# Kernel optimization log

Hardware: AMD Instinct MI355X
Metric: run time of the kernel (lower is better)

Reference implementation:

```python
import jax, jax.numpy as jnp
import numpy as np

N, E = 50000, 800000
VOCAB, D, H, EDIM = 10000, 128, 8, 16
C = D // H  # per-head channels = 16
NEG_SLOPE_ATT = 0.2   # GATv2 attention leaky_relu slope
NEG_SLOPE_OUT = 0.01  # F.leaky_relu default
BN_EPS = 1e-5


def setup_inputs() -> dict:
    key = jax.random.key(0)
    ks = jax.random.split(key, 10)
    g = lambda k, shape, fan: (jax.random.normal(k, shape, jnp.float32) / np.float32(np.sqrt(fan)))
    return {
        "x": jax.random.randint(ks[0], (N,), 0, VOCAB),
        "ei": jax.random.randint(ks[1], (2, E), 0, N),
        "ew": jax.random.normal(ks[2], (E, EDIM), jnp.float32),
        "emb": g(ks[3], (VOCAB, D), D),
        "W_l": g(ks[4], (D, D), D),
        "b_l": jnp.zeros((D,), jnp.float32),
        "W_r": g(ks[5], (D, D), D),
        "b_r": jnp.zeros((D,), jnp.float32),
        "att": g(ks[6], (H, C), C),
        "W_e": g(ks[7], (EDIM, D), EDIM),
        "bias": jnp.zeros((D,), jnp.float32),
        "gamma": jnp.ones((D,), jnp.float32),
        "beta": jnp.zeros((D,), jnp.float32),
    }


def reference(x, ei, ew, emb, W_l, b_l, W_r, b_r, att, W_e, bias, gamma, beta):
    n = x.shape[0]
    # Embeddings: lut(x) * sqrt(d_model); dropout=0 (identity)
    h = emb[x] * jnp.float32(np.sqrt(D))                      # [N, D]
    # GATv2Conv linear transforms (source / target)
    xl = (h @ W_l + b_l).reshape(n, H, C)                      # [N, H, C]
    xr = (h @ W_r + b_r).reshape(n, H, C)                      # [N, H, C]
    eemb = (ew @ W_e).reshape(-1, H, C)                        # [E, H, C]
    src, dst = ei[0], ei[1]
    # per-edge attention logits: a^T LeakyReLU(x_l[j] + x_r[i] + e)
    m = jax.nn.leaky_relu(xl[src] + xr[dst] + eemb, NEG_SLOPE_ATT)  # [E, H, C]
    score = jnp.einsum('ehc,hc->eh', m, att)                   # [E, H]
    # segment softmax over incoming edges of each target node
    smax = jax.ops.segment_max(score, dst, num_segments=n)     # [N, H]
    ex = jnp.exp(score - smax[dst])                            # [E, H]
    denom = jax.ops.segment_sum(ex, dst, num_segments=n)       # [N, H]
    alpha = ex / denom[dst]                                    # [E, H]
    # scatter-add aggregation of weighted source features
    agg = jax.ops.segment_sum(alpha[:, :, None] * xl[src], dst, num_segments=n)
    out = agg.reshape(n, D) + bias                             # [N, D]
    # BatchNorm1d (training mode: batch statistics, biased variance)
    mean = out.mean(axis=0)
    var = out.var(axis=0)
    y = (out - mean) * jax.lax.rsqrt(var + BN_EPS) * gamma + beta
    return jax.nn.leaky_relu(y, NEG_SLOPE_OUT)
```

## Files before the change

kernel.cpp:

```cpp
#include <hip/hip_runtime.h>
#include <hip/hip_bf16.h>
#include <hip/hip_fp16.h>

typedef __hip_bfloat16 bf16;
typedef unsigned short u16;

#define D 128
#define EDIM 16
#define SQRT_D 11.313708498984761f

typedef short bf16x8 __attribute__((ext_vector_type(8)));
typedef float f32x4 __attribute__((ext_vector_type(4)));
typedef _Float16 h2 __attribute__((ext_vector_type(2)));

#define PF_BL    0
#define PF_BR    128
#define PF_WE    256
#define PF_ATT   2304
#define PF_BIAS  2432
#define PF_GAMMA 2560
#define PF_BETA  2688
#define PF_TOTAL 2816

__device__ __forceinline__ u16 f2bf_bits(float f) {
    union { bf16 h; u16 s; } cv; cv.h = __float2bfloat16(f); return cv.s;
}
__device__ __forceinline__ float2 h2f2(unsigned u) {
    union { unsigned u; __half2 h; } cv; cv.u = u;
    return __half22float2(cv.h);
}
__device__ __forceinline__ int swid(int nn, int k) {
    return nn * 128 + ((((k >> 3) ^ (nn & 15)) << 3) | (k & 7));
}
__device__ __forceinline__ float red8(float x) {
    x += __int_as_float(__builtin_amdgcn_update_dpp(0, __float_as_int(x), 0xB1, 0xf, 0xf, true));
    x += __int_as_float(__builtin_amdgcn_update_dpp(0, __float_as_int(x), 0x4E, 0xf, 0xf, true));
    x += __int_as_float(__builtin_amdgcn_update_dpp(0, __float_as_int(x), 0x141, 0xf, 0xf, true));
    return x;
}

__global__ void k_zero_detect(int* p, int count, const u16* __restrict__ u, int* flag)
{
    int i = blockIdx.x * blockDim.x + threadIdx.x;
    if (i < count) p[i] = 0;
    if (blockIdx.x == 0) {
        __shared__ int sh[256];
        int t = threadIdx.x;
        int cnt = 0;
        for (int k = t; k < 4096; k += 256) {
            int e = (u[k] >> 7) & 0xFF;
            cnt += (e > 132 && e < 255) ? 1 : 0;
        }
        sh[t] = cnt;
        __syncthreads();
        for (int s = 128; s > 0; s >>= 1) {
            if (t < s) sh[t] += sh[t + s];
            __syncthreads();
        }
        if (t == 0) *flag = (sh[0] > 100) ? 1 : 0;
    }
}

__device__ __forceinline__ float rdv(const void* p, int i, int fl) {
    return fl ? ((const float*)p)[i] : __bfloat162float(((const bf16*)p)[i]);
}

__global__ __launch_bounds__(256) void k_prep_hist(
    const void* emb, const void* Wl, const void* Wr,
    const void* bl, const void* br, const void* We, const void* att,
    const void* bias, const void* gamma, const void* beta,
    const int* __restrict__ flag, u16* __restrict__ emb16,
    u16* __restrict__ WT, float* __restrict__ pf,
    const int* __restrict__ ei, int* __restrict__ deg,
    int nE, int embCount, int prepBlocks)
{
    if ((int)blockIdx.x >= prepBlocks) {
        int e = (blockIdx.x - prepBlocks) * 256 + threadIdx.x;
        if (e < nE) atomicAdd(&deg[ei[nE + e]], 1);
        return;
    }
    const int fl = *flag;
    int idx = blockIdx.x * 256 + threadIdx.x;
    const int embV = (embCount + 7) >> 3;
    if (idx < embV) {
        int base = idx << 3;
        int lim = min(8, embCount - base);
        if (lim == 8) {
            u16 o[8];
            if (fl) {
                float f[8];
                const float4* s = (const float4*)((const float*)emb + base);
                *(float4*)(f)     = s[0];
                *(float4*)(f + 4) = s[1];
                #pragma unroll
                for (int k = 0; k < 8; ++k) o[k] = f2bf_bits(f[k] * SQRT_D);
            } else {
                u16 uu[8];
                *(uint4*)uu = *(const uint4*)((const u16*)emb + base);
                #pragma unroll
                for (int k = 0; k < 8; ++k) {
                    float v = __uint_as_float(((unsigned)uu[k]) << 16);
                    o[k] = f2bf_bits(v * SQRT_D);
                }
            }
            *(uint4*)(emb16 + base) = *(uint4*)o;
        } else {
            for (int k = 0; k < lim; ++k)
                emb16[base + k] = f2bf_bits(rdv(emb, base + k, fl) * SQRT_D);
        }
        return;
    }
    idx -= embV;
    if (idx < 32768) {
        int w = idx >> 14;
        int j = idx & 16383;
        int k = j >> 7, nn = j & 127;
        const void* W = w ? Wr : Wl;
        WT[w * 16384 + swid(nn, k)] = f2bf_bits(rdv(W, k * D + nn, fl));
        return;
    }
    idx -= 32768;
    if (idx < 128)  { pf[PF_BL + idx] = rdv(bl, idx, fl); return; }
    idx -= 128;
    if (idx < 128)  { pf[PF_BR + idx] = rdv(br, idx, fl); return; }
    idx -= 128;
    if (idx < 2048) { pf[PF_WE + idx] = rdv(We, idx, fl); return; }
    idx -= 2048;
    if (idx < 128)  { pf[PF_ATT + idx] = rdv(att, idx, fl); return; }
    idx -= 128;
    if (idx < 128)  { pf[PF_BIAS + idx] = rdv(bias, idx, fl); return; }
    idx -= 128;
    if (idx < 128)  { pf[PF_GAMMA + idx] = rdv(gamma, idx, fl); return; }
    idx -= 128;
    if (idx < 128)  { pf[PF_BETA + idx] = rdv(beta, idx, fl); return; }
}

__global__ __launch_bounds__(1024) void k_scan1(
    const int* __restrict__ deg, int* __restrict__ row_ptr,
    int* __restrict__ cursor, int n, int nBlk)
{
    __shared__ int chsum[512];
    __shared__ int part[1024];
    __shared__ int myOff;
    const int t = threadIdx.x;
    const int wv = t >> 6;
    const int lane = t & 63;

    for (int c = wv; c < nBlk; c += 16) {
        int base = c << 10;
        int s = 0;
        for (int k = lane; k < 1024; k += 64) {
            int i = base + k;
            s += (i < n) ? deg[i] : 0;
        }
        #pragma unroll
        for (int m = 1; m < 64; m <<= 1) s += __shfl_xor(s, m);
        if (lane == 0) chsum[c] = s;
    }
    __syncthreads();
    if (t == 0) {
        int run = 0;
        for (int c = 0; c < (int)blockIdx.x; ++c) run += chsum[c];
        myOff = run;
    }
    __syncthreads();

    int i = blockIdx.x * 1024 + t;
    int v = (i < n) ? deg[i] : 0;
    part[t] = v;
    __syncthreads();
    for (int off = 1; off < 1024; off <<= 1) {
        int u = (t >= off) ? part[t - off] : 0;
        __syncthreads();
        part[t] += u;
        __syncthreads();
    }
    if (i < n) {
        int excl = myOff + part[t] - v;
        row_ptr[i] = excl;
        cursor[i] = excl;
        if (i == n - 1) row_ptr[n] = excl + v;
    }
}

__global__ __launch_bounds__(1024) void k_scan_sum(
    const int* __restrict__ deg, int* __restrict__ blkSum, int n)
{
    __shared__ int sh[1024];
    int t = threadIdx.x;
    int i = blockIdx.x * 1024 + t;
    sh[t] = (i < n) ? deg[i] : 0;
    __syncthreads();
    for (int s = 512; s > 0; s >>= 1) {
        if (t < s) sh[t] += sh[t + s];
        __syncthreads();
    }
    if (t == 0) blkSum[blockIdx.x] = sh[0];
}
__global__ __launch_bounds__(1024) void k_scan_blk(
    const int* __restrict__ blkSum, int* __restrict__ blkOff, int nBlk)
{
    __shared__ int part[1024];
    int t = threadIdx.x;
    int v = (t < nBlk) ? blkSum[t] : 0;
    part[t] = v;
    __syncthreads();
    for (int off = 1; off < 1024; off <<= 1) {
        int u = (t >= off) ? part[t - off] : 0;
        __syncthreads();
        part[t] += u;
        __syncthreads();
    }
    if (t < nBlk) blkOff[t] = part[t] - v;
}
__global__ __launch_bounds__(1024) void k_scan_write(
    const int* __restrict__ deg, const int* __restrict__ blkOff,
    int* __restrict__ row_ptr, int* __restrict__ cursor, int n)
{
    __shared__ int part[1024];
    int t = threadIdx.x;
    int i = blockIdx.x * 1024 + t;
    int v = (i < n) ? deg[i] : 0;
    part[t] = v;
    __syncthreads();
    for (int off = 1; off < 1024; off <<= 1) {
        int u = (t >= off) ? part[t - off] : 0;
        __syncthreads();
        part[t] += u;
        __syncthreads();
    }
    if (i < n) {
        int excl = blkOff[blockIdx.x] + part[t] - v;
        row_ptr[i] = excl;
        cursor[i] = excl;
        if (i == n - 1) row_ptr[n] = excl + v;
    }
}

__global__ __launch_bounds__(256) void k_scatter(
    const int* __restrict__ ei, int* __restrict__ cursor,
    int* __restrict__ csr, const void* __restrict__ ew,
    u16* __restrict__ ewc, const int* __restrict__ flag, int nE)
{
    int e = blockIdx.x * blockDim.x + threadIdx.x;
    if (e >= nE) return;
    int src = ei[e], dst = ei[nE + e];
    int pos = atomicAdd(&cursor[dst], 1);
    csr[pos] = src << 8;
    __half2 h[8];
    if (*flag) {
        const float4* s = (const float4*)((const float*)ew + (size_t)e * 16);
        float f[16];
        *(float4*)(f)      = s[0];
        *(float4*)(f + 4)  = s[1];
        *(float4*)(f + 8)  = s[2];
        *(float4*)(f + 12) = s[3];
        #pragma unroll
        for (int q = 0; q < 8; ++q)
            h[q] = __float22half2_rn(make_float2(f[2*q], f[2*q+1]));
    } else {
        const uint4* s = (const uint4*)((const u16*)ew + (size_t)e * 16);
        unsigned uu[8];
        *(uint4*)(uu)     = s[0];
        *(uint4*)(uu + 4) = s[1];
        #pragma unroll
        for (int q = 0; q < 8; ++q) {
            float lo = __uint_as_float(uu[q] << 16);
            float hi = __uint_as_float(uu[q] & 0xffff0000u);
            h[q] = __float22half2_rn(make_float2(lo, hi));
        }
    }
    u16* d16 = ewc + ((size_t)pos << 4);
    *(uint4*)d16       = *(uint4*)&h[0];
    *(uint4*)(d16 + 8) = *(uint4*)&h[4];
}

__global__ __launch_bounds__(256) void k_node(
    const int* __restrict__ x, const u16* __restrict__ emb16,
    const u16* __restrict__ WT, const float* __restrict__ pf,
    u16* __restrict__ xl16, u16* __restrict__ xr16, int n)
{
    __shared__ u16 Bt[2][16384];
    const int t = threadIdx.x;
    {
        const uint4* s = (const uint4*)WT;
        uint4* dd = (uint4*)&Bt[0][0];
        #pragma unroll
        for (int i = 0; i < 16; ++i) dd[i * 256 + t] = s[i * 256 + t];
    }
    const int l = t & 63;
    const int wv = t >> 6;
    const int m = l & 15;
    const int quad = l >> 4;
    const int R = blockIdx.x * 64;

    int arow = R + wv * 16 + m;
    int tok = (arow < n) ? x[arow] : 0;
    const u16* ap = emb16 + (size_t)tok * D + quad * 8;
    bf16x8 afr[4];
    #pragma unroll
    for (int kk = 0; kk < 4; ++kk) afr[kk] = *(const bf16x8*)(ap + kk * 32);
    __syncthreads();

    #pragma unroll
    for (int w = 0; w < 2; ++w) {
        const float* bb = pf + (w ? PF_BR : PF_BL);
        u16* out = w ? xr16 : xl16;
        f32x4 acc[8];
        #pragma unroll
        for (int nt = 0; nt < 8; ++nt) {
            float bv = bb[nt * 16 + m];
            acc[nt] = f32x4{bv, bv, bv, bv};
        }
        #pragma unroll
        for (int kk = 0; kk < 4; ++kk) {
            #pragma unroll
            for (int nt = 0; nt < 8; ++nt) {
                int blk = (quad + 4 * kk) ^ m;
                bf16x8 bfr = *(const bf16x8*)&Bt[w][(nt * 16 + m) * 128 + blk * 8];
                acc[nt] = __builtin_amdgcn_mfma_f32_16x16x32_bf16(afr[kk], bfr, acc[nt], 0, 0, 0);
            }
        }
        #pragma unroll
        for (int nt = 0; nt < 8; ++nt) {
            int col = nt * 16 + m;
            #pragma unroll
            for (int r = 0; r < 4; ++r) {
                int row = R + wv * 16 + quad * 4 + r;
                if (row < n)
                    out[(size_t)row * D + col] =
                        __half_as_ushort(__float2half(acc[nt][r]));
            }
        }
    }
}

struct EwH {
    unsigned v[8];
    __device__ __forceinline__ void load(const u16* base, int j) {
        const uint4* q = (const uint4*)(base + ((size_t)j << 4));
        uint4 A = q[0], B = q[1];
        v[0]=A.x; v[1]=A.y; v[2]=A.z; v[3]=A.w;
        v[4]=B.x; v[5]=B.y; v[6]=B.z; v[7]=B.w;
    }
    __device__ __forceinline__ float2 pair(int q) const { return h2f2(v[q]); }
};

__global__ __launch_bounds__(256) void k_agg(
    const int* __restrict__ row_ptr, const int* __restrict__ csr,
    const u16* __restrict__ ewc, const float* __restrict__ pf,
    const u16* __restrict__ xl16, const u16* __restrict__ xr16,
    float* __restrict__ vpre, float* __restrict__ bnsum,
    float* __restrict__ bnsumsq, int n)
{
    const int t = threadIdx.x;
    const int l = t & 63;
    const int wv = __builtin_amdgcn_readfirstlane(t >> 6);

#if __has_builtin(__builtin_amdgcn_fdot2)
    h2 we0[8], we1[8];
    #pragma unroll
    for (int q = 0; q < 8; ++q) {
        float2 a = *(const float2*)&pf[PF_WE + (2*q)   * D + 2 * l];
        float2 b = *(const float2*)&pf[PF_WE + (2*q+1) * D + 2 * l];
        we0[q] = h2{(_Float16)a.x, (_Float16)b.x};
        we1[q] = h2{(_Float16)a.y, (_Float16)b.y};
    }
#else
    float2 we[EDIM];
    #pragma unroll
    for (int k = 0; k < EDIM; ++k)
        we[k] = *(const float2*)&pf[PF_WE + k * D + 2 * l];
#endif
    const float2 attv  = *(const float2*)&pf[PF_ATT + 2 * l];
    const float2 biasv = *(const float2*)&pf[PF_BIAS + 2 * l];

    float s0 = 0, s20 = 0, s1 = 0, s21 = 0;

    const int slot = blockIdx.x * 4 + wv;
    const int i0 = slot * 4;
    const int i1 = min(i0 + 4, n);

    if (i0 < n) {
        const char* xlB = (const char*)xl16 + 4 * l;
        const char* xrB = (const char*)xr16 + 4 * l;

        int cur = i0;
        int endCur  = row_ptr[i0 + 1];
        int endNext = row_ptr[min(i0 + 2, i1)];
        const int begAll = row_ptr[i0];
        const int endAll = row_ptr[i1];

        float2 xrvCur  = h2f2(*(const unsigned*)(xrB + ((size_t)i0 << 8)));
        int nxt0 = min(i0 + 1, i1 - 1);
        float2 xrvNext = h2f2(*(const unsigned*)(xrB + ((size_t)nxt0 << 8)));

        float acc0 = 0, acc1 = 0, den = 0;

        auto finalize = [&]() {
            float inv = den > 0.f ? 1.0f / den : 0.0f;
            float v0 = fmaf(acc0, inv, biasv.x);
            float v1 = fmaf(acc1, inv, biasv.y);
            *(float2*)(vpre + ((size_t)cur << 7) + 2 * l) = make_float2(v0, v1);
            s0 += v0; s20 += v0 * v0;
            s1 += v1; s21 += v1 * v1;
            acc0 = acc1 = den = 0.f;
        };
        auto advance = [&]() {
            finalize();
            ++cur;
            endCur  = endNext;
            endNext = row_ptr[min(cur + 2, i1)];
            xrvCur  = xrvNext;
            int nxt = min(cur + 1, i1 - 1);
            xrvNext = h2f2(*(const unsigned*)(xrB + ((size_t)nxt << 8)));
        };
        auto comp = [&](const EwH& w, unsigned xbits) {
            float e0 = xrvCur.x, e1 = xrvCur.y;
#if __has_builtin(__builtin_amdgcn_fdot2)
            #pragma unroll
            for (int q = 0; q < 8; ++q) {
                h2 pr = __builtin_bit_cast(h2, w.v[q]);
                e0 = __builtin_amdgcn_fdot2(pr, we0[q], e0, false);
                e1 = __builtin_amdgcn_fdot2(pr, we1[q], e1, false);
            }
#else
            #pragma unroll
            for (int q = 0; q < 8; ++q) {
                float2 pr = w.pair(q);
                e0 = fmaf(pr.x, we[2*q].x,   e0);
                e0 = fmaf(pr.y, we[2*q+1].x, e0);
                e1 = fmaf(pr.x, we[2*q].y,   e1);
                e1 = fmaf(pr.y, we[2*q+1].y, e1);
            }
#endif
            float2 xc = h2f2(xbits);
            float z0 = xc.x + e0, z1 = xc.y + e1;
            float m0 = fmaxf(z0, 0.2f * z0);
            float m1 = fmaxf(z1, 0.2f * z1);
            float p = red8(fmaf(m1, attv.y, m0 * attv.x));
            float ex = __expf(p);
            den += ex;
            acc0 = fmaf(ex, xc.x, acc0);
            acc1 = fmaf(ex, xc.y, acc1);
        };

        const int cnt = endAll - begAll;
        if (cnt > 0) {
            EwH wA, wB, wC, wD, wE, wF;
            unsigned xA = 0, xB = 0, xC = 0, xD = 0, xE = 0, xF = 0;
            {            wA.load(ewc, begAll);     xA = *(const unsigned*)(xlB + csr[begAll]); }
            if (cnt > 1) { wB.load(ewc, begAll + 1); xB = *(const unsigned*)(xlB + csr[begAll + 1]); }
            if (cnt > 2) { wC.load(ewc, begAll + 2); xC = *(const unsigned*)(xlB + csr[begAll + 2]); }
            if (cnt > 3) { wD.load(ewc, begAll + 3); xD = *(const unsigned*)(xlB + csr[begAll + 3]); }
            if (cnt > 4) { wE.load(ewc, begAll + 4); xE = *(const unsigned*)(xlB + csr[begAll + 4]); }
            if (cnt > 5) { wF.load(ewc, begAll + 5); xF = *(const unsigned*)(xlB + csr[begAll + 5]); }

            int j  = begAll;
            int jp = begAll + 6;
            while (true) {
#define STAGE(W, X)                                                              \
                while (j >= endCur) advance();                                   \
                comp(W, X);                                                      \
                if (jp < endAll) {                                               \
                    W.load(ewc, jp);                                             \
                    X = *(const unsigned*)(xlB + csr[jp]);                       \
                }                                                                \
                ++jp; ++j;                                                       \
                if (j >= endAll) break;
                STAGE(wA, xA)
                STAGE(wB, xB)
                STAGE(wC, xC)
                STAGE(wD, xD)
                STAGE(wE, xE)
                STAGE(wF, xF)
#undef STAGE
            }
        }
        while (cur < i1) { finalize(); ++cur; }
    }

    __shared__ float sh[4][D], sh2[4][D];
    sh[wv][2*l] = s0;   sh[wv][2*l+1] = s1;
    sh2[wv][2*l] = s20; sh2[wv][2*l+1] = s21;
    __syncthreads();
    if (t < D) {
        float a = 0, a2 = 0;
        #pragma unroll
        for (int q = 0; q < 4; ++q) { a += sh[q][t]; a2 += sh2[q][t]; }
        atomicAdd(&bnsum[t], a);
        atomicAdd(&bnsumsq[t], a2);
    }
}

__global__ __launch_bounds__(256) void k_final(
    const float* __restrict__ vpre, const float* __restrict__ pf,
    const float* __restrict__ bnsum, const float* __restrict__ bnsumsq,
    float* __restrict__ out, int n)
{
    int idx = blockIdx.x * 256 + threadIdx.x;
    if (idx >= n * (D / 4)) return;
    int pos = idx * 4;
    int d = pos & (D - 1);
    const float invN = 1.0f / (float)n;
    float4 v  = *(const float4*)(vpre + pos);
    float4 ms = *(const float4*)(bnsum + d);
    float4 m2 = *(const float4*)(bnsumsq + d);
    float4 g  = *(const float4*)(pf + PF_GAMMA + d);
    float4 bt = *(const float4*)(pf + PF_BETA + d);
    float* vv = (float*)&v; float* msv = (float*)&ms; float* m2v = (float*)&m2;
    float* gv = (float*)&g; float* btv = (float*)&bt;
    float4 o;
    float* ov = (float*)&o;
    #pragma unroll
    for (int c = 0; c < 4; ++c) {
        float mean = msv[c] * invN;
        float var = m2v[c] * invN - mean * mean;
        float y = (vv[c] - mean) * rsqrtf(var + 1e-5f) * gv[c] + btv[c];
        ov[c] = y > 0.f ? y : 0.01f * y;
    }
    *(float4*)(out + pos) = o;
}

extern "C" void kernel_launch(void* const* d_in, const int* in_sizes, int n_in,
                              void* d_out, int out_size, void* d_ws, size_t ws_size,
                              hipStream_t stream)
{
    const int*  x     = (const int*)d_in[0];
    const int*  ei    = (const int*)d_in[1];
    const void* ew    = d_in[2];
    const void* emb   = d_in[3];
    const void* Wl    = d_in[4];
    const void* bl    = d_in[5];
    const void* Wr    = d_in[6];
    const void* br    = d_in[7];
    const void* att   = d_in[8];
    const void* We    = d_in[9];
    const void* bias  = d_in[10];
    const void* gamma = d_in[11];
    const void* beta  = d_in[12];

    const int n  = in_sizes[0];
    const int nE = in_sizes[1] / 2;
    const int embCount = in_sizes[3];

    const int nScanBlk = (n + 1023) / 1024;

    float* ws      = (float*)d_ws;
    float* vpre    = ws;
    u16*   xl16    = (u16*)(vpre + (size_t)n * D);
    u16*   xr16    = xl16 + (size_t)n * D;
    int*   deg     = (int*)(xr16 + (size_t)n * D);
    float* bnsum   = (float*)(deg + n);
    float* bnsumsq = bnsum + D;
    int*   flag    = (int*)(bnsumsq + D);
    int*   row_ptr = flag + 1;
    int*   cursor  = row_ptr + (n + 1);
    int*   blkSum  = cursor + n;
    int*   blkOff  = blkSum + nScanBlk;
    uintptr_t p    = (uintptr_t)(blkOff + nScanBlk);
    p = (p + 15) & ~(uintptr_t)15;
    int*   csr     = (int*)p;
    p = (uintptr_t)(csr + nE);
    p = (p + 15) & ~(uintptr_t)15;
    u16*   emb16   = (u16*)p;
    p = (uintptr_t)(emb16 + embCount);
    p = (p + 15) & ~(uintptr_t)15;
    u16*   WT      = (u16*)p;
    p = (uintptr_t)(WT + 32768);
    float* pf      = (float*)p;
    p = (uintptr_t)(pf + PF_TOTAL);
    p = (p + 15) & ~(uintptr_t)15;
    u16*   ewc     = (u16*)p;

    int zc = n + 2 * D;
    k_zero_detect<<<(zc + 255) / 256, 256, 0, stream>>>(deg, zc, (const u16*)emb, flag);

    int embV = (embCount + 7) >> 3;
    int prepN = embV + 32768 + PF_TOTAL;
    int prepBlocks = (prepN + 255) / 256;
    int histBlocks = (nE + 255) / 256;
    k_prep_hist<<<prepBlocks + histBlocks, 256, 0, stream>>>(
        emb, Wl, Wr, bl, br, We, att, bias, gamma, beta,
        flag, emb16, WT, pf, ei, deg, nE, embCount, prepBlocks);

    if (nScanBlk <= 512) {
        k_scan1<<<nScanBlk, 1024, 0, stream>>>(deg, row_ptr, cursor, n, nScanBlk);
    } else {
        k_scan_sum<<<nScanBlk, 1024, 0, stream>>>(deg, blkSum, n);
        k_scan_blk<<<1, 1024, 0, stream>>>(blkSum, blkOff, nScanBlk);
        k_scan_write<<<nScanBlk, 1024, 0, stream>>>(deg, blkOff, row_ptr, cursor, n);
    }

    k_scatter<<<histBlocks, 256, 0, stream>>>(ei, cursor, csr, ew, ewc, flag, nE);

    k_node<<<(n + 63) / 64, 256, 0, stream>>>(x, emb16, WT, pf, xl16, xr16, n);

    int aggBlocks = (n + 15) / 16;
    k_agg<<<aggBlocks, 256, 0, stream>>>(row_ptr, csr, ewc, pf, xl16, xr16,
                                         vpre, bnsum, bnsumsq, n);

    k_final<<<(n * (D / 4) + 255) / 256, 256, 0, stream>>>(
        vpre, pf, bnsum, bnsumsq, (float*)d_out, n);
}
```

Before: 362.1 us.

## Fold embedding scale into weights, fuse scatter and node GEMM kernels

Drops the separate full-vocabulary bf16 embedding conversion and instead folds the sqrt(D) scale into the transposed weights, gathering raw embedding rows directly in the node GEMM. The edge scatter and node GEMM are merged into one launch with 512-thread blocks, and the GEMM stages one weight matrix in shared memory at a time to halve LDS use. The aggregation prefetch depth drops from six edges to four. These cut a launch and a pass over the embedding table, but the extra barriers and shallower prefetch may expose latency. Applying the scale before bf16 rounding of the weights also changes rounding slightly.

Result: faster. 348.6 us (-3.7%).

```diff
diff --git a/kernel.cpp b/kernel.cpp
--- a/kernel.cpp
+++ b/kernel.cpp
@@ -66,13 +66,13 @@
 }
 
 __global__ __launch_bounds__(256) void k_prep_hist(
-    const void* emb, const void* Wl, const void* Wr,
+    const void* Wl, const void* Wr,
     const void* bl, const void* br, const void* We, const void* att,
     const void* bias, const void* gamma, const void* beta,
-    const int* __restrict__ flag, u16* __restrict__ emb16,
+    const int* __restrict__ flag,
     u16* __restrict__ WT, float* __restrict__ pf,
     const int* __restrict__ ei, int* __restrict__ deg,
-    int nE, int embCount, int prepBlocks)
+    int nE, int prepBlocks)
 {
     if ((int)blockIdx.x >= prepBlocks) {
         int e = (blockIdx.x - prepBlocks) * 256 + threadIdx.x;
@@ -81,42 +81,12 @@
     }
     const int fl = *flag;
     int idx = blockIdx.x * 256 + threadIdx.x;
-    const int embV = (embCount + 7) >> 3;
-    if (idx < embV) {
-        int base = idx << 3;
-        int lim = min(8, embCount - base);
-        if (lim == 8) {
-            u16 o[8];
-            if (fl) {
-                float f[8];
-                const float4* s = (const float4*)((const float*)emb + base);
-                *(float4*)(f)     = s[0];
-                *(float4*)(f + 4) = s[1];
-                #pragma unroll
-                for (int k = 0; k < 8; ++k) o[k] = f2bf_bits(f[k] * SQRT_D);
-            } else {
-                u16 uu[8];
-                *(uint4*)uu = *(const uint4*)((const u16*)emb + base);
-                #pragma unroll
-                for (int k = 0; k < 8; ++k) {
-                    float v = __uint_as_float(((unsigned)uu[k]) << 16);
-                    o[k] = f2bf_bits(v * SQRT_D);
-                }
-            }
-            *(uint4*)(emb16 + base) = *(uint4*)o;
-        } else {
-            for (int k = 0; k < lim; ++k)
-                emb16[base + k] = f2bf_bits(rdv(emb, base + k, fl) * SQRT_D);
-        }
-        return;
-    }
-    idx -= embV;
     if (idx < 32768) {
         int w = idx >> 14;
         int j = idx & 16383;
         int k = j >> 7, nn = j & 127;
         const void* W = w ? Wr : Wl;
-        WT[w * 16384 + swid(nn, k)] = f2bf_bits(rdv(W, k * D + nn, fl));
+        WT[w * 16384 + swid(nn, k)] = f2bf_bits(rdv(W, k * D + nn, fl) * SQRT_D);
         return;
     }
     idx -= 32768;
@@ -237,73 +207,87 @@
     }
 }
 
-__global__ __launch_bounds__(256) void k_scatter(
+__global__ __launch_bounds__(512) void k_scatnode(
     const int* __restrict__ ei, int* __restrict__ cursor,
     int* __restrict__ csr, const void* __restrict__ ew,
-    u16* __restrict__ ewc, const int* __restrict__ flag, int nE)
-{
-    int e = blockIdx.x * blockDim.x + threadIdx.x;
-    if (e >= nE) return;
-    int src = ei[e], dst = ei[nE + e];
-    int pos = atomicAdd(&cursor[dst], 1);
-    csr[pos] = src << 8;
-    __half2 h[8];
-    if (*flag) {
-        const float4* s = (const float4*)((const float*)ew + (size_t)e * 16);
-        float f[16];
-        *(float4*)(f)      = s[0];
-        *(float4*)(f + 4)  = s[1];
-        *(float4*)(f + 8)  = s[2];
-        *(float4*)(f + 12) = s[3];
-        #pragma unroll
-        for (int q = 0; q < 8; ++q)
-            h[q] = __float22half2_rn(make_float2(f[2*q], f[2*q+1]));
-    } else {
-        const uint4* s = (const uint4*)((const u16*)ew + (size_t)e * 16);
-        unsigned uu[8];
-        *(uint4*)(uu)     = s[0];
-        *(uint4*)(uu + 4) = s[1];
-        #pragma unroll
-        for (int q = 0; q < 8; ++q) {
-            float lo = __uint_as_float(uu[q] << 16);
-            float hi = __uint_as_float(uu[q] & 0xffff0000u);
-            h[q] = __float22half2_rn(make_float2(lo, hi));
-        }
-    }
-    u16* d16 = ewc + ((size_t)pos << 4);
-    *(uint4*)d16       = *(uint4*)&h[0];
-    *(uint4*)(d16 + 8) = *(uint4*)&h[4];
-}
-
-__global__ __launch_bounds__(256) void k_node(
-    const int* __restrict__ x, const u16* __restrict__ emb16,
+    u16* __restrict__ ewc, const int* __restrict__ flag, int nE,
+    const int* __restrict__ x, const void* __restrict__ emb,
     const u16* __restrict__ WT, const float* __restrict__ pf,
-    u16* __restrict__ xl16, u16* __restrict__ xr16, int n)
-{
-    __shared__ u16 Bt[2][16384];
+    u16* __restrict__ xl16, u16* __restrict__ xr16, int n, int scatBlocks)
+{
+    __shared__ u16 Bt[16384];
     const int t = threadIdx.x;
-    {
-        const uint4* s = (const uint4*)WT;
-        uint4* dd = (uint4*)&Bt[0][0];
-        #pragma unroll
-        for (int i = 0; i < 16; ++i) dd[i * 256 + t] = s[i * 256 + t];
-    }
+
+    if ((int)blockIdx.x < scatBlocks) {
+        int e = blockIdx.x * 512 + t;
+        if (e >= nE) return;
+        int src = ei[e], dst = ei[nE + e];
+        int pos = atomicAdd(&cursor[dst], 1);
+        csr[pos] = src << 8;
+        __half2 h[8];
+        if (*flag) {
+            const float4* s = (const float4*)((const float*)ew + (size_t)e * 16);
+            float f[16];
+            *(float4*)(f)      = s[0];
+            *(float4*)(f + 4)  = s[1];
+            *(float4*)(f + 8)  = s[2];
+            *(float4*)(f + 12) = s[3];
+            #pragma unroll
+            for (int q = 0; q < 8; ++q)
+                h[q] = __float22half2_rn(make_float2(f[2*q], f[2*q+1]));
+        } else {
+            const uint4* s = (const uint4*)((const u16*)ew + (size_t)e * 16);
+            unsigned uu[8];
+            *(uint4*)(uu)     = s[0];
+            *(uint4*)(uu + 4) = s[1];
+            #pragma unroll
+            for (int q = 0; q < 8; ++q) {
+                float lo = __uint_as_float(uu[q] << 16);
+                float hi = __uint_as_float(uu[q] & 0xffff0000u);
+                h[q] = __float22half2_rn(make_float2(lo, hi));
+            }
+        }
+        u16* d16 = ewc + ((size_t)pos << 4);
+        *(uint4*)d16       = *(uint4*)&h[0];
+        *(uint4*)(d16 + 8) = *(uint4*)&h[4];
+        return;
+    }
+
+    const int fl = *flag;
     const int l = t & 63;
     const int wv = t >> 6;
     const int m = l & 15;
     const int quad = l >> 4;
-    const int R = blockIdx.x * 64;
+    const int R = (blockIdx.x - scatBlocks) * 128;
 
     int arow = R + wv * 16 + m;
     int tok = (arow < n) ? x[arow] : 0;
-    const u16* ap = emb16 + (size_t)tok * D + quad * 8;
     bf16x8 afr[4];
-    #pragma unroll
-    for (int kk = 0; kk < 4; ++kk) afr[kk] = *(const bf16x8*)(ap + kk * 32);
-    __syncthreads();
+    if (!fl) {
+        const u16* ap = (const u16*)emb + (size_t)tok * D + quad * 8;
+        #pragma unroll
+        for (int kk = 0; kk < 4; ++kk) afr[kk] = *(const bf16x8*)(ap + kk * 32);
+    } else {
+        const float* ap = (const float*)emb + (size_t)tok * D + quad * 8;
+        #pragma unroll
+        for (int kk = 0; kk < 4; ++kk) {
+            float4 a = *(const float4*)(ap + kk * 32);
+            float4 b = *(const float4*)(ap + kk * 32 + 4);
+            u16 o[8] = { f2bf_bits(a.x), f2bf_bits(a.y), f2bf_bits(a.z), f2bf_bits(a.w),
+                         f2bf_bits(b.x), f2bf_bits(b.y), f2bf_bits(b.z), f2bf_bits(b.w) };
+            afr[kk] = *(bf16x8*)o;
+        }
+    }
 
     #pragma unroll
     for (int w = 0; w < 2; ++w) {
+        {
+            const uint4* s = (const uint4*)(WT + w * 16384);
+            uint4* dd = (uint4*)&Bt[0];
+            #pragma unroll
+            for (int i = 0; i < 4; ++i) dd[i * 512 + t] = s[i * 512 + t];
+        }
+        __syncthreads();
         const float* bb = pf + (w ? PF_BR : PF_BL);
         u16* out = w ? xr16 : xl16;
         f32x4 acc[8];
@@ -317,7 +301,7 @@
             #pragma unroll
             for (int nt = 0; nt < 8; ++nt) {
                 int blk = (quad + 4 * kk) ^ m;
-                bf16x8 bfr = *(const bf16x8*)&Bt[w][(nt * 16 + m) * 128 + blk * 8];
+                bf16x8 bfr = *(const bf16x8*)&Bt[(nt * 16 + m) * 128 + blk * 8];
                 acc[nt] = __builtin_amdgcn_mfma_f32_16x16x32_bf16(afr[kk], bfr, acc[nt], 0, 0, 0);
             }
         }
@@ -332,6 +316,7 @@
                         __half_as_ushort(__float2half(acc[nt][r]));
             }
         }
+        __syncthreads();
     }
 }
 
@@ -447,17 +432,15 @@
 
         const int cnt = endAll - begAll;
         if (cnt > 0) {
-            EwH wA, wB, wC, wD, wE, wF;
-            unsigned xA = 0, xB = 0, xC = 0, xD = 0, xE = 0, xF = 0;
+            EwH wA, wB, wC, wD;
+            unsigned xA = 0, xB = 0, xC = 0, xD = 0;
             {            wA.load(ewc, begAll);     xA = *(const unsigned*)(xlB + csr[begAll]); }
             if (cnt > 1) { wB.load(ewc, begAll + 1); xB = *(const unsigned*)(xlB + csr[begAll + 1]); }
             if (cnt > 2) { wC.load(ewc, begAll + 2); xC = *(const unsigned*)(xlB + csr[begAll + 2]); }
             if (cnt > 3) { wD.load(ewc, begAll + 3); xD = *(const unsigned*)(xlB + csr[begAll + 3]); }
-            if (cnt > 4) { wE.load(ewc, begAll + 4); xE = *(const unsigned*)(xlB + csr[begAll + 4]); }
-            if (cnt > 5) { wF.load(ewc, begAll + 5); xF = *(const unsigned*)(xlB + csr[begAll + 5]); }
 
             int j  = begAll;
-            int jp = begAll + 6;
+            int jp = begAll + 4;
             while (true) {
 #define STAGE(W, X)                                                              \
                 while (j >= endCur) advance();                                   \
@@ -472,8 +455,6 @@
                 STAGE(wB, xB)
                 STAGE(wC, xC)
                 STAGE(wD, xD)
-                STAGE(wE, xE)
-                STAGE(wF, xF)
 #undef STAGE
             }
         }
@@ -542,7 +523,6 @@
 
     const int n  = in_sizes[0];
     const int nE = in_sizes[1] / 2;
-    const int embCount = in_sizes[3];
 
     const int nScanBlk = (n + 1023) / 1024;
 
@@ -563,9 +543,6 @@
     int*   csr     = (int*)p;
     p = (uintptr_t)(csr + nE);
     p = (p + 15) & ~(uintptr_t)15;
-    u16*   emb16   = (u16*)p;
-    p = (uintptr_t)(emb16 + embCount);
-    p = (p + 15) & ~(uintptr_t)15;
     u16*   WT      = (u16*)p;
     p = (uintptr_t)(WT + 32768);
     float* pf      = (float*)p;
@@ -576,13 +553,12 @@
     int zc = n + 2 * D;
     k_zero_detect<<<(zc + 255) / 256, 256, 0, stream>>>(deg, zc, (const u16*)emb, flag);
 
-    int embV = (embCount + 7) >> 3;
-    int prepN = embV + 32768 + PF_TOTAL;
+    int prepN = 32768 + PF_TOTAL;
     int prepBlocks = (prepN + 255) / 256;
     int histBlocks = (nE + 255) / 256;
     k_prep_hist<<<prepBlocks + histBlocks, 256, 0, stream>>>(
-        emb, Wl, Wr, bl, br, We, att, bias, gamma, beta,
-        flag, emb16, WT, pf, ei, deg, nE, embCount, prepBlocks);
+        Wl, Wr, bl, br, We, att, bias, gamma, beta,
+        flag, WT, pf, ei, deg, nE, prepBlocks);
 
     if (nScanBlk <= 512) {
         k_scan1<<<nScanBlk, 1024, 0, stream>>>(deg, row_ptr, cursor, n, nScanBlk);
@@ -592,9 +568,11 @@
         k_scan_write<<<nScanBlk, 1024, 0, stream>>>(deg, blkOff, row_ptr, cursor, n);
     }
 
-    k_scatter<<<histBlocks, 256, 0, stream>>>(ei, cursor, csr, ew, ewc, flag, nE);
-
-    k_node<<<(n + 63) / 64, 256, 0, stream>>>(x, emb16, WT, pf, xl16, xr16, n);
+    int scatBlocks = (nE + 511) / 512;
+    int nodeBlocks = (n + 127) / 128;
+    k_scatnode<<<scatBlocks + nodeBlocks, 512, 0, stream>>>(
+        ei, cursor, csr, ew, ewc, flag, nE,
+        x, emb, WT, pf, xl16, xr16, n, scatBlocks);
 
     int aggBlocks = (n + 15) / 16;
     k_agg<<<aggBlocks, 256, 0, stream>>>(row_ptr, csr, ewc, pf, xl16, xr16,
```
